# Kernel tuning notes

Hardware: AMD Instinct MI355X
Metric: run time of the kernel (lower is better)

Reference implementation:

```python
import jax, jax.numpy as jnp
import numpy as np

EMB_DIM = 16
N_DIM = 20
P_DIM = 10
VOCAB = 32000
B = 2048
T = 24
DIST_FACTOR = 1.0
M_ISOM = EMB_DIM * (EMB_DIM - 1) // 2  # 120


def make_embed_index(d):
    idx = []
    for i in range(1, d + 1):
        for j in range(i + 1, d + 1):
            idx.append([d * (i - 1) + i - 1, d * (i - 1) + j - 1,
                        d * (j - 1) + i - 1, d * (j - 1) + j - 1])
    return np.asarray(idx, dtype=np.int32)  # [m, 4]

EMBED_INDEX = jnp.asarray(make_embed_index(EMB_DIM))


def sym(x):
    return 0.5 * (x + jnp.swapaxes(x, -1, -2))


def sym_funcm(x, f):
    # f applied to eigenvalues of symmetric x
    w, v = jnp.linalg.eigh(x)
    return jnp.einsum('...ij,...j,...kj->...ik', v, f(w), v)


def cayley_map(x):
    eye = jnp.eye(x.shape[-1], dtype=x.dtype)
    return (eye - x) @ jnp.linalg.inv(eye + x)


def tangent_vector(x):
    p, q = x.shape
    n = p + q
    a = jnp.zeros((n, n), x.dtype)
    a = a.at[:p, p:].set(x)
    return a.at[p:, :p].set(-x.T)


def tangent_vector_batch(x):
    b, t, p, q = x.shape
    n = p + q
    a = jnp.zeros((b, t, n, n), x.dtype)
    a = a.at[:, :, :p, p:].set(x)
    return a.at[:, :, p:, :p].set(-jnp.swapaxes(x, 2, 3))


def addition_tangents(x):
    # x: [B, T, d, d] symmetric tangents; sequential SPD 'addition'
    y0 = sym_funcm(x[:, -1], jnp.exp)                         # [B, d, d]
    s = sym_funcm(x[:, :-1], lambda t: jnp.exp(0.5 * t))      # [B, T-1, d, d]
    s_rev = jnp.flip(jnp.swapaxes(s, 0, 1), axis=0)           # [T-1, B, d, d]
    def step(y, si):
        return si @ y @ si, None
    y, _ = jax.lax.scan(step, y0, s_rev)
    return y


def addition_point_tangent(x, t):
    y = sym_funcm(t, jnp.exp)
    sqrt_x = sym_funcm(x, jnp.sqrt)
    return sqrt_x @ y @ sqrt_x


def dist_spd(a, b):
    inv_sqrt_a = sym_funcm(a, lambda w: 1.0 / jnp.sqrt(w))
    m = sym(inv_sqrt_a @ b @ inv_sqrt_a)
    log_eigvals = jnp.log(jnp.linalg.eigvalsh(m))
    # Riemannian (affine-invariant) metric: ||log eigvals||_2
    return jnp.sqrt(jnp.sum(log_eigvals * log_eigvals, axis=-1))  # [B]


def addition_tangents_gr(x, base_point):
    # x: [B, T, n, n] skew tangents
    y = cayley_map(x)                                # [B, T, n, n]
    def step(z, yi):
        return z @ yi, None
    z, _ = jax.lax.scan(step, y[:, 0], jnp.swapaxes(y[:, 1:], 0, 1))
    return z @ base_point @ jnp.linalg.inv(z)


def build_rel_isometry(ref_params):
    # ref_params: [1, m] rotation angles -> product of m Givens-like rotations
    ang = ref_params[0]
    src = jnp.stack([jnp.cos(ang), -jnp.sin(ang), jnp.sin(ang), jnp.cos(ang)], axis=-1)  # [m,4]
    flat = jnp.tile(jnp.eye(EMB_DIM, dtype=src.dtype).reshape(1, EMB_DIM * EMB_DIM), (M_ISOM, 1))
    flat = flat.at[jnp.arange(M_ISOM)[:, None], EMBED_INDEX].set(src)
    rots = flat.reshape(M_ISOM, EMB_DIM, EMB_DIM)
    def step(acc, r):
        return acc @ r, None
    rel, _ = jax.lax.scan(step, rots[0], rots[1:])
    return rel  # [d, d]


def setup_inputs():
    key = jax.random.key(0)
    ks = jax.random.split(key, 10)
    return {
        'question_ids': jax.random.randint(ks[0], (B, T), 0, VOCAB),
        'answer_ids': jax.random.randint(ks[1], (B, T), 0, VOCAB),
        'question_embedding_spd': jax.random.normal(ks[2], (VOCAB, EMB_DIM, EMB_DIM), jnp.float32) * 1e-3,
        'answer_embedding_spd': jax.random.normal(ks[3], (VOCAB, EMB_DIM, EMB_DIM), jnp.float32) * 1e-3,
        'ref_params': jax.random.uniform(ks[4], (1, M_ISOM), jnp.float32) * 0.5 - 0.25,
        'question_bias_spd': jax.random.uniform(ks[5], (EMB_DIM, EMB_DIM), jnp.float32) * 2.0 - 1.0,
        'question_embedding_gr': jax.random.normal(ks[6], (VOCAB, P_DIM, N_DIM - P_DIM), jnp.float32) * 1e-3,
        'answer_embedding_gr': jax.random.normal(ks[7], (VOCAB, P_DIM, N_DIM - P_DIM), jnp.float32) * 1e-3,
        'question_transforms_gr': jax.random.uniform(ks[8], (P_DIM, N_DIM - P_DIM), jnp.float32) * 2.0 - 1.0,
        'question_bias_gr': jax.random.uniform(ks[9], (P_DIM, N_DIM - P_DIM), jnp.float32) * 2.0 - 1.0,
        'wf': jnp.float32(1.0),
        'wb': jnp.float32(1.0),
    }


def reference(question_ids, answer_ids, question_embedding_spd, answer_embedding_spd,
              ref_params, question_bias_spd, question_embedding_gr, answer_embedding_gr,
              question_transforms_gr, question_bias_gr, wf, wb):
    # ---- SPD branch ----
    q_bias = sym(question_bias_spd)
    q_tok = sym(question_embedding_spd[question_ids])        # [B, T, d, d]
    q_spd = addition_tangents(q_tok)                          # [B, d, d]
    rel = build_rel_isometry(ref_params)                      # [d, d]
    q_spd = rel @ q_spd @ rel.T
    q_spd = addition_point_tangent(q_spd, q_bias)
    a_tok = sym(answer_embedding_spd[answer_ids])
    a_spd = addition_tangents(a_tok)
    d_spd = dist_spd(q_spd, a_spd)                            # [B]
    # ---- Grassmannian branch ----
    base_point = jnp.diag(jnp.concatenate([jnp.ones(P_DIM, jnp.float32),
                                           jnp.zeros(N_DIM - P_DIM, jnp.float32)]))
    bias_gr = tangent_vector(question_bias_gr)                # [n, n]
    q_gr_tok = tangent_vector_batch(question_transforms_gr * question_embedding_gr[question_ids])
    q_gr = addition_tangents_gr(q_gr_tok, base_point)         # [B, n, n]
    y_bias = cayley_map(bias_gr)
    q_gr = y_bias @ q_gr @ jnp.linalg.inv(y_bias)
    a_gr_tok = tangent_vector_batch(answer_embedding_gr[answer_ids])
    a_gr = addition_tangents_gr(a_gr_tok, base_point)
    diff = q_gr - a_gr
    d_gr = jnp.sqrt(jnp.sum(diff * diff, axis=(1, 2)))        # [B]
    dist = DIST_FACTOR * d_spd + d_gr
    return -wf * dist + wb
```

## Files before the change

kernel.cpp:

```cpp
#include <hip/hip_runtime.h>
#include <hip/hip_bf16.h>

#define NBATCH 2048
#define NTOK 24
#define NS_ITERS 2
#define JSWEEPS 4
#define SP 28

__device__ __forceinline__ float bf2f(unsigned short u) {
  union { unsigned int i; float f; } v;
  v.i = ((unsigned int)u) << 16;
  return v.f;
}

__device__ __forceinline__ float ldin(const void* p, long idx, bool f32) {
  return f32 ? ((const float*)p)[idx] : bf2f(((const unsigned short*)p)[idx]);
}

__device__ __forceinline__ bool detect_f32(const void* wfp) {
  return *((const unsigned int*)wfp) == 0x3F800000u;
}

__device__ __forceinline__ void wsync() {
  __asm__ volatile("s_waitcnt lgkmcnt(0)" ::: "memory");
}

template<bool BT>
__device__ __forceinline__ void mmS(const float* A, const float* B, float* C,
                                    float alpha, float beta, float pa) {
  const int lane = threadIdx.x & 63;
  const int i = lane >> 2;
  const int j0 = (lane & 3) << 2;
  float a0 = 0.f, a1 = 0.f, a2 = 0.f, a3 = 0.f;
  float o0 = 0.f, o1 = 0.f, o2 = 0.f, o3 = 0.f;
#pragma unroll
  for (int k4 = 0; k4 < 4; ++k4) {
    const float4 av = *(const float4*)(A + i * SP + k4 * 4);
    if ((lane & 3) == k4) { o0 = av.x; o1 = av.y; o2 = av.z; o3 = av.w; }
    if (!BT) {
      const float4 b0 = *(const float4*)(B + (k4 * 4 + 0) * SP + j0);
      const float4 b1 = *(const float4*)(B + (k4 * 4 + 1) * SP + j0);
      const float4 b2 = *(const float4*)(B + (k4 * 4 + 2) * SP + j0);
      const float4 b3 = *(const float4*)(B + (k4 * 4 + 3) * SP + j0);
      a0 += av.x * b0.x + av.y * b1.x + av.z * b2.x + av.w * b3.x;
      a1 += av.x * b0.y + av.y * b1.y + av.z * b2.y + av.w * b3.y;
      a2 += av.x * b0.z + av.y * b1.z + av.z * b2.z + av.w * b3.z;
      a3 += av.x * b0.w + av.y * b1.w + av.z * b2.w + av.w * b3.w;
    } else {
      const float4 r0 = *(const float4*)(B + (j0 + 0) * SP + k4 * 4);
      const float4 r1 = *(const float4*)(B + (j0 + 1) * SP + k4 * 4);
      const float4 r2 = *(const float4*)(B + (j0 + 2) * SP + k4 * 4);
      const float4 r3 = *(const float4*)(B + (j0 + 3) * SP + k4 * 4);
      a0 += av.x * r0.x + av.y * r0.y + av.z * r0.z + av.w * r0.w;
      a1 += av.x * r1.x + av.y * r1.y + av.z * r1.z + av.w * r1.w;
      a2 += av.x * r2.x + av.y * r2.y + av.z * r2.z + av.w * r2.w;
      a3 += av.x * r3.x + av.y * r3.y + av.z * r3.z + av.w * r3.w;
    }
  }
  wsync();
  *(float4*)(C + i * SP + j0) = float4{
      alpha * a0 + ((i == j0 + 0) ? beta : 0.f) + pa * o0,
      alpha * a1 + ((i == j0 + 1) ? beta : 0.f) + pa * o1,
      alpha * a2 + ((i == j0 + 2) ? beta : 0.f) + pa * o2,
      alpha * a3 + ((i == j0 + 3) ? beta : 0.f) + pa * o3};
  wsync();
}

__device__ __forceinline__ void mmS_btg(const float* A, const float* B,
                                        float* __restrict__ G) {
  const int lane = threadIdx.x & 63;
  const int i = lane >> 2;
  const int j0 = (lane & 3) << 2;
  float a0 = 0.f, a1 = 0.f, a2 = 0.f, a3 = 0.f;
#pragma unroll
  for (int k4 = 0; k4 < 4; ++k4) {
    const float4 av = *(const float4*)(A + i * SP + k4 * 4);
    const float4 r0 = *(const float4*)(B + (j0 + 0) * SP + k4 * 4);
    const float4 r1 = *(const float4*)(B + (j0 + 1) * SP + k4 * 4);
    const float4 r2 = *(const float4*)(B + (j0 + 2) * SP + k4 * 4);
    const float4 r3 = *(const float4*)(B + (j0 + 3) * SP + k4 * 4);
    a0 += av.x * r0.x + av.y * r0.y + av.z * r0.z + av.w * r0.w;
    a1 += av.x * r1.x + av.y * r1.y + av.z * r1.z + av.w * r1.w;
    a2 += av.x * r2.x + av.y * r2.y + av.z * r2.z + av.w * r2.w;
    a3 += av.x * r3.x + av.y * r3.y + av.z * r3.z + av.w * r3.w;
  }
  *(float4*)(G + i * 16 + j0) = float4{a0, a1, a2, a3};
}

__device__ __forceinline__ float dot12(const float* a, const float* b) {
  float s = 0.f;
#pragma unroll
  for (int m = 0; m < 3; ++m) {
    const float4 x = *(const float4*)(a + 4 * m);
    const float4 y = *(const float4*)(b + 4 * m);
    s += x.x * y.x + x.y * y.y + x.z * y.z + x.w * y.w;
  }
  return s;
}
__device__ __forceinline__ float dot24(const float* a, const float* b) {
  float s = 0.f;
#pragma unroll
  for (int m = 0; m < 6; ++m) {
    const float4 x = *(const float4*)(a + 4 * m);
    const float4 y = *(const float4*)(b + 4 * m);
    s += x.x * y.x + x.y * y.y + x.z * y.z + x.w * y.w;
  }
  return s;
}

__device__ __forceinline__ int gpos(int e) {
  const int c = e / 20, i = e % 20;
  return c * 24 + (i < 10 ? i : i + 2);
}
__device__ __forceinline__ float grel(const float* MR, const float* MTn,
                                      const float* VT, int e) {
  const int c = e / 20, i = e % 20;
  return (i < 10) ? dot12(MR + i * 12, VT + c * 24 + 12)
                  : dot12(MTn + (i - 10) * 12, VT + c * 24);
}

__host__ __device__ constexpr int jpart(int idx, int r) {
  if (idx == 15) return r;
  int d = idx - r; d = (d % 15 + 15) % 15;
  if (d == 0) return 15;
  int p = (2 * r - idx) % 15;
  return (p + 15) % 15;
}

__device__ __forceinline__ void mm16o(const float* A, const float* B, float* C,
                                      float alpha, float beta) {
  const int lane = threadIdx.x & 63;
  const int i = lane >> 2;
  const int j0 = (lane & 3) << 2;
  float a0 = 0.f, a1 = 0.f, a2 = 0.f, a3 = 0.f;
#pragma unroll
  for (int k4 = 0; k4 < 4; ++k4) {
    const float4 av = *(const float4*)(A + i * 16 + k4 * 4);
    const float4 b0 = *(const float4*)(B + (k4 * 4 + 0) * 16 + j0);
    const float4 b1 = *(const float4*)(B + (k4 * 4 + 1) * 16 + j0);
    const float4 b2 = *(const float4*)(B + (k4 * 4 + 2) * 16 + j0);
    const float4 b3 = *(const float4*)(B + (k4 * 4 + 3) * 16 + j0);
    a0 += av.x * b0.x + av.y * b1.x + av.z * b2.x + av.w * b3.x;
    a1 += av.x * b0.y + av.y * b1.y + av.z * b2.y + av.w * b3.y;
    a2 += av.x * b0.z + av.y * b1.z + av.z * b2.z + av.w * b3.z;
    a3 += av.x * b0.w + av.y * b1.w + av.z * b2.w + av.w * b3.w;
  }
  wsync();
  C[i * 16 + j0 + 0] = alpha * a0 + ((i == j0 + 0) ? beta : 0.f);
  C[i * 16 + j0 + 1] = alpha * a1 + ((i == j0 + 1) ? beta : 0.f);
  C[i * 16 + j0 + 2] = alpha * a2 + ((i == j0 + 2) ? beta : 0.f);
  C[i * 16 + j0 + 3] = alpha * a3 + ((i == j0 + 3) ? beta : 0.f);
  wsync();
}

__global__ void __launch_bounds__(256) k_setup(
    const void* __restrict__ refp, const void* __restrict__ biasspd,
    const void* __restrict__ biasgr, const void* __restrict__ wfp,
    float* __restrict__ wsRel, float* __restrict__ wsEm, float* __restrict__ wsYbp) {
  __shared__ __align__(16) float sm[2656];
  const int t = threadIdx.x;
  const int w = t >> 6;
  const int lane = t & 63;
  const bool f32 = detect_f32(wfp);

  float* RELT = sm;
  float* caA  = sm + 256;
  float* saA  = sm + 376;
  float* Zb   = sm + 512;
  float* Tb   = sm + 768;
  float* AUG  = sm + 1024;
  float* IMX  = sm + 1824;
  float* YBs  = sm + 2224;
  float* SF   = sm + 2624;

  if (w == 0) {
    {
      const float a0 = ldin(refp, lane < 120 ? lane : 0, f32);
      if (lane < 120) { caA[lane] = cosf(a0); saA[lane] = sinf(a0); }
      if (lane < 56) {
        const float a1 = ldin(refp, lane + 64, f32);
        caA[lane + 64] = cosf(a1); saA[lane + 64] = sinf(a1);
      }
    }
#pragma unroll
    for (int r = 0; r < 4; ++r) {
      const int idx = lane + 64 * r;
      RELT[idx] = ((idx >> 4) == (idx & 15)) ? 1.f : 0.f;
    }
    wsync();
    int m = 0;
    for (int a = 0; a < 16; ++a) {
      for (int bc = a + 1; bc < 16; ++bc, ++m) {
        const float ca = caA[m], sa = saA[m];
        if (lane < 16) {
          const float u = RELT[a * 16 + lane];
          const float v = RELT[bc * 16 + lane];
          RELT[a * 16 + lane] = ca * u + sa * v;
          RELT[bc * 16 + lane] = -sa * u + ca * v;
        }
        wsync();
      }
    }
#pragma unroll
    for (int r = 0; r < 4; ++r) {
      const int idx = lane + 64 * r;
      wsRel[idx] = RELT[(idx & 15) * 16 + (idx >> 4)];
    }
  } else if (w == 1) {
#pragma unroll
    for (int r = 0; r < 4; ++r) {
      const int idx = lane + 64 * r;
      Tb[idx] = ldin(biasspd, idx, f32);
    }
    wsync();
#pragma unroll
    for (int r = 0; r < 4; ++r) {
      const int idx = lane + 64 * r;
      const int i = idx >> 4, j = idx & 15;
      Zb[idx] = -(Tb[idx] + Tb[j * 16 + i]) * (0.5f / 128.f);
    }
    wsync();
#pragma unroll
    for (int r = 0; r < 4; ++r) {
      const int idx = lane + 64 * r;
      const int i = idx >> 4, j = idx & 15;
      Tb[idx] = Zb[idx] * (1.f / 6.f) + ((i == j) ? 1.f : 0.f);
    }
    wsync();
    mm16o(Zb, Tb, Tb, 1.f / 5.f, 1.f);
    mm16o(Zb, Tb, Tb, 1.f / 4.f, 1.f);
    mm16o(Zb, Tb, Tb, 1.f / 3.f, 1.f);
    mm16o(Zb, Tb, Tb, 1.f / 2.f, 1.f);
    mm16o(Zb, Tb, Tb, 1.f, 1.f);
    for (int sq = 0; sq < 6; ++sq) mm16o(Tb, Tb, Tb, 1.f, 0.f);
#pragma unroll
    for (int r = 0; r < 4; ++r) {
      const int idx = lane + 64 * r;
      wsEm[idx] = Tb[idx];
    }
  } else if (w == 2) {
    for (int idx = lane; idx < 800; idx += 64) {
      const int r = idx / 40, c = idx % 40;
      float v;
      if (c < 20) {
        float xb = 0.f;
        if (r < 10 && c >= 10) xb = ldin(biasgr, r * 10 + (c - 10), f32);
        else if (r >= 10 && c < 10) xb = -ldin(biasgr, c * 10 + (r - 10), f32);
        v = xb + ((r == c) ? 1.f : 0.f);
      } else {
        v = ((c - 20) == r) ? 1.f : 0.f;
      }
      AUG[idx] = v;
    }
    for (int idx = lane; idx < 400; idx += 64) {
      const int r = idx / 20, c = idx % 20;
      float xb = 0.f;
      if (r < 10 && c >= 10) xb = ldin(biasgr, r * 10 + (c - 10), f32);
      else if (r >= 10 && c < 10) xb = -ldin(biasgr, c * 10 + (r - 10), f32);
      IMX[idx] = ((r == c) ? 1.f : 0.f) - xb;
    }
    wsync();
    for (int k = 0; k < 20; ++k) {
      const float pinv = 1.f / AUG[k * 40 + k];
      wsync();
      if (lane < 40) AUG[k * 40 + lane] *= pinv;
      wsync();
      if (lane < 20) SF[lane] = AUG[lane * 40 + k];
      wsync();
      for (int idx = lane; idx < 800; idx += 64) {
        const int r = idx / 40, c = idx % 40;
        if (r != k) AUG[idx] -= SF[r] * AUG[k * 40 + c];
      }
      wsync();
    }
    {
      float o0 = 0.f, o1 = 0.f, o2 = 0.f, o3 = 0.f, o4 = 0.f, o5 = 0.f, o6 = 0.f;
#pragma unroll
      for (int kk = 0; kk < 20; ++kk) {
        const float* ar = AUG + kk * 40 + 20;
        o0 += IMX[(lane) / 20 * 20 + kk] * ar[(lane) % 20];
        o1 += IMX[(lane + 64) / 20 * 20 + kk] * ar[(lane + 64) % 20];
        o2 += IMX[(lane + 128) / 20 * 20 + kk] * ar[(lane + 128) % 20];
        o3 += IMX[(lane + 192) / 20 * 20 + kk] * ar[(lane + 192) % 20];
        o4 += IMX[(lane + 256) / 20 * 20 + kk] * ar[(lane + 256) % 20];
        o5 += IMX[(lane + 320) / 20 * 20 + kk] * ar[(lane + 320) % 20];
        if (lane < 16) o6 += IMX[(lane + 384) / 20 * 20 + kk] * ar[(lane + 384) % 20];
      }
      wsync();
      YBs[lane] = o0; YBs[lane + 64] = o1; YBs[lane + 128] = o2;
      YBs[lane + 192] = o3; YBs[lane + 256] = o4; YBs[lane + 320] = o5;
      if (lane < 16) YBs[lane + 384] = o6;
      wsync();
    }
    for (int s = lane; s < 480; s += 64) {
      const int i = s / 24, sl = s % 24;
      float v = 0.f;
      if (sl < 10) v = YBs[i * 20 + sl];
      else if (sl >= 12 && sl < 22) v = YBs[i * 20 + (sl - 2)];
      wsYbp[s] = v;
    }
  }
}

__global__ void __launch_bounds__(64) k_work(
    const int* __restrict__ qids, const int* __restrict__ aids,
    const void* __restrict__ qemb, const void* __restrict__ aemb,
    const void* __restrict__ qembg, const void* __restrict__ aembg,
    const void* __restrict__ transg, const void* __restrict__ wfp,
    const float* __restrict__ wsRel, const float* __restrict__ wsYbp,
    float* __restrict__ wsQ1, float* __restrict__ wsSA,
    float* __restrict__ wsWQ, float* __restrict__ wsWA) {
  __shared__ __align__(16) float sm[1600];
  const int lane = threadIdx.x;
  const bool f32 = detect_f32(wfp);
  const int bid = blockIdx.x;
  const int type = bid >> 11;
  const int b = bid & (NBATCH - 1);

  if (type >= 2) {
    const bool isq = (type == 2);
    float* T = sm;
    float* Z = sm + 448;
    float* C = sm + 896;
    float* E = sm + 1344;
    const int i4 = lane >> 2;
    const int j4 = (lane & 3) << 2;
    if (isq) {
      *(float4*)(C + i4 * SP + j4) = *(const float4*)(wsRel + 4 * lane);
    } else {
      *(float4*)(C + i4 * SP + j4) = float4{
          (i4 == j4 + 0) ? 1.f : 0.f, (i4 == j4 + 1) ? 1.f : 0.f,
          (i4 == j4 + 2) ? 1.f : 0.f, (i4 == j4 + 3) ? 1.f : 0.f};
    }
    wsync();
    const int* ids = isq ? qids : aids;
    const void* emb = isq ? qemb : aemb;
    int idbuf[NTOK];
#pragma unroll
    for (int t = 0; t < NTOK; ++t) idbuf[t] = ids[b * NTOK + t];
    const int gs[5] = {0, 6, 12, 18, 23};
#pragma unroll
    for (int g = 0; g < 4; ++g) {
      const int gb = gs[g], ge = gs[g + 1];
      float e0 = 0.f, e1 = 0.f, e2 = 0.f, e3 = 0.f;
      if (f32) {
        float4 vv[6];
#pragma unroll
        for (int u = 0; u < 6; ++u)
          if (gb + u < ge)
            vv[u] = *(const float4*)((const float*)emb + (size_t)idbuf[gb + u] * 256 + 4 * lane);
#pragma unroll
        for (int u = 0; u < 6; ++u)
          if (gb + u < ge) { e0 += vv[u].x; e1 += vv[u].y; e2 += vv[u].z; e3 += vv[u].w; }
      } else {
        uint2 uu[6];
#pragma unroll
        for (int u = 0; u < 6; ++u)
          if (gb + u < ge)
            uu[u] = *(const uint2*)((const unsigned short*)emb + (size_t)idbuf[gb + u] * 256 + 4 * lane);
#pragma unroll
        for (int u = 0; u < 6; ++u)
          if (gb + u < ge) {
            e0 += bf2f((unsigned short)(uu[u].x & 0xffffu));
            e1 += bf2f((unsigned short)(uu[u].x >> 16));
            e2 += bf2f((unsigned short)(uu[u].y & 0xffffu));
            e3 += bf2f((unsigned short)(uu[u].y >> 16));
          }
      }
      *(float4*)(E + 4 * lane) = float4{e0, e1, e2, e3};
      wsync();
      const float t0 = E[(j4 + 0) * 16 + i4];
      const float t1 = E[(j4 + 1) * 16 + i4];
      const float t2 = E[(j4 + 2) * 16 + i4];
      const float t3 = E[(j4 + 3) * 16 + i4];
      *(float4*)(Z + i4 * SP + j4) = float4{
          0.25f * (e0 + t0), 0.25f * (e1 + t1),
          0.25f * (e2 + t2), 0.25f * (e3 + t3)};
      wsync();
      mmS<false>(C, Z, C, 1.f, 0.f, 1.f);
    }
    {
      float e0, e1, e2, e3;
      if (f32) {
        const float4 v = *(const float4*)((const float*)emb + (size_t)idbuf[NTOK - 1] * 256 + 4 * lane);
        e0 = v.x; e1 = v.y; e2 = v.z; e3 = v.w;
      } else {
        const uint2 v = *(const uint2*)((const unsigned short*)emb + (size_t)idbuf[NTOK - 1] * 256 + 4 * lane);
        e0 = bf2f((unsigned short)(v.x & 0xffffu));
        e1 = bf2f((unsigned short)(v.x >> 16));
        e2 = bf2f((unsigned short)(v.y & 0xffffu));
        e3 = bf2f((unsigned short)(v.y >> 16));
      }
      *(float4*)(E + 4 * lane) = float4{e0, e1, e2, e3};
      wsync();
      const float t0 = E[(j4 + 0) * 16 + i4];
      const float t1 = E[(j4 + 1) * 16 + i4];
      const float t2 = E[(j4 + 2) * 16 + i4];
      const float t3 = E[(j4 + 3) * 16 + i4];
      *(float4*)(Z + i4 * SP + j4) = float4{
          0.25f * (e0 + t0), 0.25f * (e1 + t1),
          0.25f * (e2 + t2), 0.25f * (e3 + t3)};
      wsync();
      mmS<false>(Z, Z, Z, 2.f, 1.f, 2.f);
    }
    mmS<false>(C, Z, T, 1.f, 0.f, 0.f);
    mmS_btg(T, C, (isq ? wsQ1 : wsSA) + (size_t)b * 256);
  } else {
    const bool isq = (type == 0);
    float* VT  = sm;
    float* OUT = sm + 240;
    float* Mr  = sm + 480;
    float* MR  = sm + 584;
    float* MTn = sm + 704;
    float* YBl = sm + 824;
    float tr0 = 1.f, tr1 = 1.f;
    if (isq) {
      tr0 = ldin(transg, lane, f32);
      tr1 = (lane < 36) ? ldin(transg, lane + 64, f32) : 0.f;
      for (int s = lane; s < 480; s += 64) YBl[s] = wsYbp[s];
    }
    for (int s = lane; s < 240; s += 64) {
      const int c = s / 24, sl = s % 24;
      VT[s] = (sl < 10 && sl == c) ? 1.f : 0.f;
    }
    wsync();
    const int* ids = isq ? qids : aids;
    const void* eg = isq ? qembg : aembg;
    int idbuf[NTOK];
#pragma unroll
    for (int t = 0; t < NTOK; ++t) idbuf[t] = ids[b * NTOK + t];
#pragma unroll
    for (int g = 0; g < 4; ++g) {
      float a0[6], a1[6];
#pragma unroll
      for (int u = 0; u < 6; ++u) {
        const size_t off = (size_t)idbuf[23 - 6 * g - u] * 100;
        a0[u] = ldin(eg, off + lane, f32);
        a1[u] = (lane < 36) ? ldin(eg, off + lane + 64, f32) : 0.f;
      }
      float m0 = 0.f, m1 = 0.f;
#pragma unroll
      for (int u = 0; u < 6; ++u) { m0 += a0[u]; m1 += a1[u]; }
      if (isq) { m0 *= tr0; m1 *= tr1; }
      Mr[lane] = m0;
      if (lane < 36) Mr[lane + 64] = m1;
      wsync();
#pragma unroll
      for (int r = 0; r < 2; ++r) {
        const int s = lane + 64 * r;
        if (s < 120) {
          const int i = s / 12, k = s % 12;
          MR[s]  = (k < 10) ? Mr[i * 10 + k] : 0.f;
          MTn[s] = (k < 10) ? -Mr[k * 10 + i] : 0.f;
        }
      }
      wsync();
      {
        const int p0 = gpos(lane), p1 = gpos(lane + 64), p2 = gpos(lane + 128);
        const int p3g = (lane < 8) ? gpos(lane + 192) : 0;
        const float s0 = grel(MR, MTn, VT, lane);
        const float s1 = grel(MR, MTn, VT, lane + 64);
        const float s2 = grel(MR, MTn, VT, lane + 128);
        const float s3 = (lane < 8) ? grel(MR, MTn, VT, lane + 192) : 0.f;
        const float v0 = VT[p0] - 2.f * s0;
        const float v1 = VT[p1] - 2.f * s1;
        const float v2 = VT[p2] - 2.f * s2;
        const float v3 = (lane < 8) ? VT[p3g] - 2.f * s3 : 0.f;
        wsync();
        VT[p0] = v0; VT[p1] = v1; VT[p2] = v2;
        if (lane < 8) VT[p3g] = v3;
        wsync();
      }
    }
    if (isq) {
      const float s0 = dot24(YBl + (lane % 20) * 24, VT + (lane / 20) * 24);
      const float s1 = dot24(YBl + ((lane + 64) % 20) * 24, VT + ((lane + 64) / 20) * 24);
      const float s2 = dot24(YBl + ((lane + 128) % 20) * 24, VT + ((lane + 128) / 20) * 24);
      const float s3 = (lane < 8) ? dot24(YBl + ((lane + 192) % 20) * 24, VT + ((lane + 192) / 20) * 24) : 0.f;
      wsync();
      OUT[gpos(lane)] = s0;
      OUT[gpos(lane + 64)] = s1;
      OUT[gpos(lane + 128)] = s2;
      if (lane < 8) OUT[gpos(lane + 192)] = s3;
      if (lane < 10) {
        OUT[lane * 24 + 10] = 0.f; OUT[lane * 24 + 11] = 0.f;
        OUT[lane * 24 + 22] = 0.f; OUT[lane * 24 + 23] = 0.f;
      }
      wsync();
      if (lane < 60)
        *(float4*)(wsWQ + (size_t)b * 240 + 4 * lane) = *(const float4*)(OUT + 4 * lane);
    } else {
      if (lane < 60)
        *(float4*)(wsWA + (size_t)b * 240 + 4 * lane) = *(const float4*)(VT + 4 * lane);
    }
  }
}

__global__ void __launch_bounds__(64) k_fin(
    const float* __restrict__ wsQ1, const float* __restrict__ wsSA,
    const float* __restrict__ wsWQ, const float* __restrict__ wsWA,
    const float* __restrict__ wsEm, const void* __restrict__ wfp,
    const void* __restrict__ wbp, void* __restrict__ outp) {
  __shared__ __align__(16) float sm[3200];
  __shared__ int prt[240];
  float* Yc = sm;
  float* Zc = sm + 448;
  float* Tm = sm + 896;
  float* SA = sm + 1344;
  float* EM = sm + 1792;
  float* G0 = sm + 2240;
  float* WQT = sm + 2688;
  float* WAT = sm + 2928;
  float* csn = sm + 3168;
  const int lane = threadIdx.x;
  const int b = blockIdx.x;
  const bool f32 = detect_f32(wfp);
  const int i4 = lane >> 2, j4 = (lane & 3) << 2;

  *(float4*)(Yc + i4 * SP + j4) = *(const float4*)(wsQ1 + (size_t)b * 256 + 4 * lane);
  *(float4*)(SA + i4 * SP + j4) = *(const float4*)(wsSA + (size_t)b * 256 + 4 * lane);
  *(float4*)(EM + i4 * SP + j4) = *(const float4*)(wsEm + 4 * lane);
  *(float4*)(Zc + i4 * SP + j4) = float4{
      (i4 == j4 + 0) ? 1.f : 0.f, (i4 == j4 + 1) ? 1.f : 0.f,
      (i4 == j4 + 2) ? 1.f : 0.f, (i4 == j4 + 3) ? 1.f : 0.f};
  if (lane < 60) {
    *(float4*)(WQT + 4 * lane) = *(const float4*)(wsWQ + (size_t)b * 240 + 4 * lane);
    *(float4*)(WAT + 4 * lane) = *(const float4*)(wsWA + (size_t)b * 240 + 4 * lane);
  }
  for (int s = lane; s < 240; s += 64) prt[s] = jpart(s & 15, s >> 4);
  wsync();

  for (int it = 0; it < NS_ITERS; ++it) {
    mmS<false>(Zc, Yc, Tm, -0.5f, 1.5f, 0.f);
    mmS<false>(Yc, Tm, Yc, 1.f, 0.f, 0.f);
    mmS<false>(Tm, Zc, Zc, 1.f, 0.f, 0.f);
  }
  mmS<false>(EM, Zc, Yc, 1.f, 0.f, 0.f);
  mmS<false>(Yc, SA, Tm, 1.f, 0.f, 0.f);
  mmS<true>(Tm, Yc, G0, 1.f, 0.f, 0.f);

  float acc = 0.f;
#pragma unroll
  for (int r = 0; r < 5; ++r) {
    const int e = lane + 64 * r;
    if (e < 300) {
      const int g = e / 100, rem = e % 100, p = rem / 10, q = rem % 10;
      const float* X = (g == 1) ? WAT : WQT;
      const float* Y = (g == 0) ? WQT : WAT;
      const float v = dot24(X + p * 24, Y + q * 24);
      acc += (g == 2) ? -2.f * v * v : v * v;
    }
  }
#pragma unroll
  for (int m = 32; m > 0; m >>= 1) acc += __shfl_xor(acc, m, 64);
  const float dgr = sqrtf(fmaxf(acc, 0.f));

  for (int sw = 0; sw < JSWEEPS; ++sw) {
    for (int r = 0; r < 15; ++r) {
      if (lane < 16) {
        const int pj = prt[r * 16 + lane];
        const int p = min(lane, pj), q = max(lane, pj);
        const float app = G0[p * SP + p], aqq = G0[q * SP + q], apq = G0[p * SP + q];
        float tau = (aqq - app) / (2.f * apq);
        float tt = 1.f / (fabsf(tau) + sqrtf(1.f + tau * tau));
        float th = (tau >= 0.f) ? tt : -tt;
        th = (fabsf(apq) > 1e-30f) ? th : 0.f;
        const float c = 1.f / sqrtf(1.f + th * th);
        const float sv = th * c;
        csn[2 * lane] = c;
        csn[2 * lane + 1] = (lane == p) ? -sv : sv;
      }
      wsync();
      {
        const int pi = prt[r * 16 + i4];
        const int pj0 = prt[r * 16 + j4 + 0];
        const int pj1 = prt[r * 16 + j4 + 1];
        const int pj2 = prt[r * 16 + j4 + 2];
        const int pj3 = prt[r * 16 + j4 + 3];
        const float2 ci = *(const float2*)(csn + 2 * i4);
        const float2 c0 = *(const float2*)(csn + 2 * (j4 + 0));
        const float2 c1 = *(const float2*)(csn + 2 * (j4 + 1));
        const float2 c2 = *(const float2*)(csn + 2 * (j4 + 2));
        const float2 c3 = *(const float2*)(csn + 2 * (j4 + 3));
        const float4 own = *(const float4*)(G0 + i4 * SP + j4);
        const float4 prw = *(const float4*)(G0 + pi * SP + j4);
        const float o0 = G0[i4 * SP + pj0];
        const float o1 = G0[i4 * SP + pj1];
        const float o2 = G0[i4 * SP + pj2];
        const float o3 = G0[i4 * SP + pj3];
        const float p0 = G0[pi * SP + pj0];
        const float p1 = G0[pi * SP + pj1];
        const float p2 = G0[pi * SP + pj2];
        const float p3 = G0[pi * SP + pj3];
        wsync();
        *(float4*)(G0 + i4 * SP + j4) = float4{
            ci.x * (c0.x * own.x + c0.y * o0) + ci.y * (c0.x * prw.x + c0.y * p0),
            ci.x * (c1.x * own.y + c1.y * o1) + ci.y * (c1.x * prw.y + c1.y * p1),
            ci.x * (c2.x * own.z + c2.y * o2) + ci.y * (c2.x * prw.z + c2.y * p2),
            ci.x * (c3.x * own.w + c3.y * o3) + ci.y * (c3.x * prw.w + c3.y * p3)};
        wsync();
      }
    }
  }

  float ss = 0.f;
  if (lane < 16) {
    const float lam = fmaxf(G0[lane * SP + lane], 1e-30f);
    const float lg = logf(lam);
    ss = lg * lg;
  }
#pragma unroll
  for (int m = 32; m > 0; m >>= 1) ss += __shfl_xor(ss, m, 64);
  if (lane == 0) {
    const float dspd = sqrtf(ss);
    const float wf = ldin(wfp, 0, f32), wb = ldin(wbp, 0, f32);
    const float val = -wf * (dspd + dgr) + wb;
    if (f32) ((float*)outp)[b] = val;
    else ((__hip_bfloat16*)outp)[b] = __float2bfloat16(val);
  }
}

extern "C" void kernel_launch(void* const* d_in, const int* in_sizes, int n_in,
                              void* d_out, int out_size, void* d_ws, size_t ws_size,
                              hipStream_t stream) {
  const int* qids = (const int*)d_in[0];
  const int* aids = (const int*)d_in[1];
  const void* qemb = d_in[2];
  const void* aemb = d_in[3];
  const void* refp = d_in[4];
  const void* biasspd = d_in[5];
  const void* qembg = d_in[6];
  const void* aembg = d_in[7];
  const void* transg = d_in[8];
  const void* biasgr = d_in[9];
  const void* wfp = d_in[10];
  const void* wbp = d_in[11];

  float* ws = (float*)d_ws;
  float* wsRel = ws;
  float* wsEm  = ws + 256;
  float* wsYbp = ws + 512;
  float* wsQ1  = ws + 1024;
  float* wsSA  = wsQ1 + (size_t)NBATCH * 256;
  float* wsWQ  = wsSA + (size_t)NBATCH * 256;
  float* wsWA  = wsWQ + (size_t)NBATCH * 240;

  k_setup<<<1, 256, 0, stream>>>(refp, biasspd, biasgr, wfp, wsRel, wsEm, wsYbp);
  k_work<<<4 * NBATCH, 64, 0, stream>>>(qids, aids, qemb, aemb, qembg, aembg,
                                        transg, wfp, wsRel, wsYbp,
                                        wsQ1, wsSA, wsWQ, wsWA);
  k_fin<<<NBATCH, 64, 0, stream>>>(wsQ1, wsSA, wsWQ, wsWA, wsEm, wfp, wbp, d_out);
}
```

Baseline: 252.9 us.

## Replace table-driven Jacobi rotations with Brent-Luk 2x2 block systolic scheme

Replaces the cyclic Jacobi eigenvalue sweep, which used a precomputed pairing table and a cos/sin array in shared memory, with a Brent-Luk style layout. Each lane owns a 2x2 block, computes the rotation for its diagonal block, gets the column rotation by shuffle, applies both sides and writes the result to permuted positions. This removes the per-round table lookups, the csn staging, one barrier per round and the scattered shared-memory gathers. The risk is that a different pairing order changes the convergence behaviour within the fixed sweep count.

New measurement: 234.1 us. 1.08x faster.

```diff
diff --git a/kernel.cpp b/kernel.cpp
--- a/kernel.cpp
+++ b/kernel.cpp
@@ -119,14 +119,6 @@
                   : dot12(MTn + (i - 10) * 12, VT + c * 24);
 }
 
-__host__ __device__ constexpr int jpart(int idx, int r) {
-  if (idx == 15) return r;
-  int d = idx - r; d = (d % 15 + 15) % 15;
-  if (d == 0) return 15;
-  int p = (2 * r - idx) % 15;
-  return (p + 15) % 15;
-}
-
 __device__ __forceinline__ void mm16o(const float* A, const float* B, float* C,
                                       float alpha, float beta) {
   const int lane = threadIdx.x & 63;
@@ -501,8 +493,7 @@
     const float* __restrict__ wsWQ, const float* __restrict__ wsWA,
     const float* __restrict__ wsEm, const void* __restrict__ wfp,
     const void* __restrict__ wbp, void* __restrict__ outp) {
-  __shared__ __align__(16) float sm[3200];
-  __shared__ int prt[240];
+  __shared__ __align__(16) float sm[3168];
   float* Yc = sm;
   float* Zc = sm + 448;
   float* Tm = sm + 896;
@@ -511,7 +502,6 @@
   float* G0 = sm + 2240;
   float* WQT = sm + 2688;
   float* WAT = sm + 2928;
-  float* csn = sm + 3168;
   const int lane = threadIdx.x;
   const int b = blockIdx.x;
   const bool f32 = detect_f32(wfp);
@@ -527,7 +517,6 @@
     *(float4*)(WQT + 4 * lane) = *(const float4*)(wsWQ + (size_t)b * 240 + 4 * lane);
     *(float4*)(WAT + 4 * lane) = *(const float4*)(wsWA + (size_t)b * 240 + 4 * lane);
   }
-  for (int s = lane; s < 240; s += 64) prt[s] = jpart(s & 15, s >> 4);
   wsync();
 
   for (int it = 0; it < NS_ITERS; ++it) {
@@ -555,51 +544,41 @@
   for (int m = 32; m > 0; m >>= 1) acc += __shfl_xor(acc, m, 64);
   const float dgr = sqrtf(fmaxf(acc, 0.f));
 
-  for (int sw = 0; sw < JSWEEPS; ++sw) {
-    for (int r = 0; r < 15; ++r) {
-      if (lane < 16) {
-        const int pj = prt[r * 16 + lane];
-        const int p = min(lane, pj), q = max(lane, pj);
-        const float app = G0[p * SP + p], aqq = G0[q * SP + q], apq = G0[p * SP + q];
-        float tau = (aqq - app) / (2.f * apq);
-        float tt = 1.f / (fabsf(tau) + sqrtf(1.f + tau * tau));
-        float th = (tau >= 0.f) ? tt : -tt;
-        th = (fabsf(apq) > 1e-30f) ? th : 0.f;
-        const float c = 1.f / sqrtf(1.f + th * th);
-        const float sv = th * c;
-        csn[2 * lane] = c;
-        csn[2 * lane + 1] = (lane == p) ? -sv : sv;
-      }
-      wsync();
-      {
-        const int pi = prt[r * 16 + i4];
-        const int pj0 = prt[r * 16 + j4 + 0];
-        const int pj1 = prt[r * 16 + j4 + 1];
-        const int pj2 = prt[r * 16 + j4 + 2];
-        const int pj3 = prt[r * 16 + j4 + 3];
-        const float2 ci = *(const float2*)(csn + 2 * i4);
-        const float2 c0 = *(const float2*)(csn + 2 * (j4 + 0));
-        const float2 c1 = *(const float2*)(csn + 2 * (j4 + 1));
-        const float2 c2 = *(const float2*)(csn + 2 * (j4 + 2));
-        const float2 c3 = *(const float2*)(csn + 2 * (j4 + 3));
-        const float4 own = *(const float4*)(G0 + i4 * SP + j4);
-        const float4 prw = *(const float4*)(G0 + pi * SP + j4);
-        const float o0 = G0[i4 * SP + pj0];
-        const float o1 = G0[i4 * SP + pj1];
-        const float o2 = G0[i4 * SP + pj2];
-        const float o3 = G0[i4 * SP + pj3];
-        const float p0 = G0[pi * SP + pj0];
-        const float p1 = G0[pi * SP + pj1];
-        const float p2 = G0[pi * SP + pj2];
-        const float p3 = G0[pi * SP + pj3];
-        wsync();
-        *(float4*)(G0 + i4 * SP + j4) = float4{
-            ci.x * (c0.x * own.x + c0.y * o0) + ci.y * (c0.x * prw.x + c0.y * p0),
-            ci.x * (c1.x * own.y + c1.y * o1) + ci.y * (c1.x * prw.y + c1.y * p1),
-            ci.x * (c2.x * own.z + c2.y * o2) + ci.y * (c2.x * prw.z + c2.y * p2),
-            ci.x * (c3.x * own.w + c3.y * o3) + ci.y * (c3.x * prw.w + c3.y * p3)};
-        wsync();
-      }
+  {
+    const int r8 = lane >> 3;
+    const int c8 = lane & 7;
+    const int sr0 = (r8 == 0) ? 0 : ((r8 == 7) ? 15 : 2 * r8 + 2);
+    const int sr1 = (r8 == 0) ? 2 : (2 * r8 - 1);
+    const int sc0 = (c8 == 0) ? 0 : ((c8 == 7) ? 15 : 2 * c8 + 2);
+    const int sc1 = (c8 == 0) ? 2 : (2 * c8 - 1);
+    for (int rd = 0; rd < JSWEEPS * 15; ++rd) {
+      const float2 t0 = *(const float2*)(G0 + (2 * r8) * SP + 2 * c8);
+      const float2 t1 = *(const float2*)(G0 + (2 * r8 + 1) * SP + 2 * c8);
+      const float2 d0 = *(const float2*)(G0 + (2 * r8) * SP + 2 * r8);
+      const float2 d1 = *(const float2*)(G0 + (2 * r8 + 1) * SP + 2 * r8);
+      const float app = d0.x, apq = d0.y, aqq = d1.y;
+      const float tau = (aqq - app) / (2.f * apq);
+      const float tt = 1.f / (fabsf(tau) + sqrtf(1.f + tau * tau));
+      float th = (tau >= 0.f) ? tt : -tt;
+      th = (fabsf(apq) > 1e-30f) ? th : 0.f;
+      const float cr_ = 1.f / sqrtf(1.f + th * th);
+      const float sr_ = th * cr_;
+      const float cc_ = __shfl(cr_, 9 * c8, 64);
+      const float sc_ = __shfl(sr_, 9 * c8, 64);
+      const float m00 = cc_ * t0.x - sc_ * t0.y;
+      const float m01 = sc_ * t0.x + cc_ * t0.y;
+      const float m10 = cc_ * t1.x - sc_ * t1.y;
+      const float m11 = sc_ * t1.x + cc_ * t1.y;
+      const float n00 = cr_ * m00 - sr_ * m10;
+      const float n01 = cr_ * m01 - sr_ * m11;
+      const float n10 = sr_ * m00 + cr_ * m10;
+      const float n11 = sr_ * m01 + cr_ * m11;
+      wsync();
+      G0[sr0 * SP + sc0] = n00;
+      G0[sr0 * SP + sc1] = n01;
+      G0[sr1 * SP + sc0] = n10;
+      G0[sr1 * SP + sc1] = n11;
+      wsync();
     }
   }
 
```
